# Optimization experiments

Measured on AMD Instinct MI355X. Metric: run time of the kernel, lower is better.

Reference implementation:

```python
import jax, jax.numpy as jnp
import numpy as np

ALPHA = 0.2  # leaky_relu negative slope
NEG_INF = -1e18


def setup_inputs() -> dict:
    key = jax.random.key(0)
    ks = jax.random.split(key, 7)
    B, N, E = 32, 1024, 768
    OUT, MLP = 256, 2
    sent_emb = jax.random.normal(ks[0], (B, N, E), dtype=jnp.float32)
    batch_e = jnp.sort(jax.random.randint(ks[1], (B, 4), 0, N), axis=-1)
    # xavier-ish scaled weights
    W_w = jax.random.normal(ks[2], (OUT, E), dtype=jnp.float32) * (1.0 / np.sqrt(E))
    W_b = jax.random.normal(ks[3], (OUT,), dtype=jnp.float32) * 0.02
    a_w = jax.random.normal(ks[4], (1, 2 * OUT), dtype=jnp.float32) * (1.0 / np.sqrt(2 * OUT))
    mlp_w = jax.random.normal(ks[5], (MLP, OUT), dtype=jnp.float32) * (1.0 / np.sqrt(OUT))
    mlp_b = jax.random.normal(ks[6], (MLP,), dtype=jnp.float32) * 0.02
    return {"sent_emb": sent_emb, "batch_e": batch_e, "W_w": W_w, "W_b": W_b,
            "a_w": a_w, "mlp_w": mlp_w, "mlp_b": mlp_b}


def reference(sent_emb, batch_e, W_w, W_b, a_w, mlp_w, mlp_b):
    B, N, E = sent_emb.shape
    OUT = W_w.shape[0]
    # Wh = W(sent_emb): [B, N, OUT]
    Wh = jnp.einsum('bne,oe->bno', sent_emb, W_w) + W_b
    # a_T([H1 || H2]) decomposes: a1 . Wh_i + a2 . Wh_j (avoids [N,N,2*OUT] concat)
    a1, a2 = a_w[0, :OUT], a_w[0, OUT:]
    s1 = Wh @ a1  # [B, N]
    s2 = Wh @ a2  # [B, N]
    e = jax.nn.leaky_relu(s1[:, :, None] + s2[:, None, :], negative_slope=ALPHA)  # [B,N,N]
    # event mask: 0.9 inside [e1s,e1e)x[e2s,e2e), 0.1 elsewhere (both > 0, kept for fidelity)
    idx = jnp.arange(N)
    row_in = (idx[None, :] >= batch_e[:, 0:1]) & (idx[None, :] < batch_e[:, 1:2])  # [B,N]
    col_in = (idx[None, :] >= batch_e[:, 2:3]) & (idx[None, :] < batch_e[:, 3:4])  # [B,N]
    event_mask = jnp.where(row_in[:, :, None] & col_in[:, None, :], 0.9, 0.1)
    masked_e = jnp.where(event_mask > 0, e, NEG_INF)
    attn = jax.nn.softmax(masked_e, axis=-1)  # [B,N,N]
    h_prime = jax.nn.elu(jnp.einsum('bnm,bmo->bno', attn, Wh))  # [B,N,OUT]
    pooled = jnp.mean(h_prime, axis=1)  # avg_pooling over nodes -> [B,OUT]
    return pooled @ mlp_w.T + mlp_b  # [B, mlp_size]
```

## Files before the change

kernel.cpp:

```cpp
#include <hip/hip_runtime.h>
#include <hip/hip_bf16.h>

#define LOG2E 1.4426950408889634f

typedef short bfrag8 __attribute__((ext_vector_type(8)));
typedef float accf4 __attribute__((ext_vector_type(4)));

__device__ __forceinline__ unsigned pack2(float a, float b) {
    __hip_bfloat162 h = __float22bfloat162_rn(make_float2(a, b));
    return *(unsigned*)&h;
}
__device__ __forceinline__ float bflo(unsigned u) { return __uint_as_float(u << 16); }
__device__ __forceinline__ float bfhi(unsigned u) { return __uint_as_float(u & 0xFFFF0000u); }

__device__ __forceinline__ void gload_lds16(const void* g, void* lds) {
    __builtin_amdgcn_global_load_lds(
        (const __attribute__((address_space(1))) unsigned int*)g,
        (__attribute__((address_space(3))) unsigned int*)lds, 16, 0, 0);
}

__global__ __launch_bounds__(256) void gemm1_kernel(
    const float* __restrict__ sent, const float* __restrict__ Ww,
    const float* __restrict__ Wb, const float* __restrict__ aw,
    unsigned short* __restrict__ WhT, float* __restrict__ s1part,
    float* __restrict__ s2part)
{
    __shared__ unsigned short SM[2][128][72];
    __shared__ float sb1[128][2];
    __shared__ float sb2[128][2];
    const int bid0 = blockIdx.x;
    const int wg = ((bid0 & 7) << 6) + (bid0 >> 3);
    const int brow = wg >> 1, bcol = wg & 1;
    const int t    = threadIdx.x;
    const int lane = t & 63, w = t >> 6;
    const int wr = w >> 1, wc = w & 1;
    const int l15 = lane & 15, l4 = lane >> 4;
    accf4 acc[4][4];
#pragma unroll
    for (int i = 0; i < 4; ++i)
#pragma unroll
        for (int j = 0; j < 4; ++j)
            acc[i][j] = (accf4){0.f, 0.f, 0.f, 0.f};
    const int r0 = t >> 3;
    const int c8 = (t & 7) << 3;

    for (int k0 = 0; k0 < 768; k0 += 64) {
#pragma unroll
        for (int i = 0; i < 4; ++i) {
            const int r = (i << 5) + r0;
            const float* ga = &sent[(size_t)(brow * 128 + r) * 768 + k0 + c8];
            float4 v0 = *(const float4*)ga;
            float4 v1 = *(const float4*)(ga + 4);
            uint4 pk;
            pk.x = pack2(v0.x, v0.y); pk.y = pack2(v0.z, v0.w);
            pk.z = pack2(v1.x, v1.y); pk.w = pack2(v1.z, v1.w);
            *(uint4*)&SM[0][r][c8] = pk;
            const float* gb = &Ww[(size_t)(bcol * 128 + r) * 768 + k0 + c8];
            float4 u0 = *(const float4*)gb;
            float4 u1 = *(const float4*)(gb + 4);
            uint4 qk;
            qk.x = pack2(u0.x, u0.y); qk.y = pack2(u0.z, u0.w);
            qk.z = pack2(u1.x, u1.y); qk.w = pack2(u1.z, u1.w);
            *(uint4*)&SM[1][r][c8] = qk;
        }
        __syncthreads();
#pragma unroll
        for (int kk = 0; kk < 2; ++kk) {
            const int ka = (kk << 5) + (l4 << 3);
            bfrag8 af[4], bfg[4];
#pragma unroll
            for (int mi = 0; mi < 4; ++mi)
                af[mi] = *(const bfrag8*)&SM[0][(wr << 6) + (mi << 4) + l15][ka];
#pragma unroll
            for (int ni = 0; ni < 4; ++ni)
                bfg[ni] = *(const bfrag8*)&SM[1][(wc << 6) + (ni << 4) + l15][ka];
#pragma unroll
            for (int mi = 0; mi < 4; ++mi)
#pragma unroll
                for (int ni = 0; ni < 4; ++ni)
                    acc[mi][ni] = __builtin_amdgcn_mfma_f32_16x16x32_bf16(
                        af[mi], bfg[ni], acc[mi][ni], 0, 0, 0);
        }
        __syncthreads();
    }

    unsigned short (*T)[136] = reinterpret_cast<unsigned short(*)[136]>(&SM[0][0][0]);
    float sp1[16], sp2[16];
#pragma unroll
    for (int i = 0; i < 16; ++i) { sp1[i] = 0.f; sp2[i] = 0.f; }
#pragma unroll
    for (int ni = 0; ni < 4; ++ni) {
        const int colL = (wc << 6) + (ni << 4) + l15;
        const int gcol = bcol * 128 + colL;
        const float wb  = Wb[gcol];
        const float a1c = aw[gcol] * LOG2E;
        const float a2c = aw[256 + gcol] * LOG2E;
#pragma unroll
        for (int mi = 0; mi < 4; ++mi) {
            const int rowL = (wr << 6) + (mi << 4) + (l4 << 2);
            float v0 = acc[mi][ni][0] + wb, v1 = acc[mi][ni][1] + wb;
            float v2 = acc[mi][ni][2] + wb, v3 = acc[mi][ni][3] + wb;
            uint2 pk; pk.x = pack2(v0, v1); pk.y = pack2(v2, v3);
            *(uint2*)&T[colL][rowL] = pk;
            sp1[mi * 4 + 0] += v0 * a1c; sp1[mi * 4 + 1] += v1 * a1c;
            sp1[mi * 4 + 2] += v2 * a1c; sp1[mi * 4 + 3] += v3 * a1c;
            sp2[mi * 4 + 0] += v0 * a2c; sp2[mi * 4 + 1] += v1 * a2c;
            sp2[mi * 4 + 2] += v2 * a2c; sp2[mi * 4 + 3] += v3 * a2c;
        }
    }
#pragma unroll
    for (int d = 1; d < 16; d <<= 1) {
#pragma unroll
        for (int i = 0; i < 16; ++i) {
            sp1[i] += __shfl_xor(sp1[i], d);
            sp2[i] += __shfl_xor(sp2[i], d);
        }
    }
    if (l15 == 0) {
#pragma unroll
        for (int mi = 0; mi < 4; ++mi)
#pragma unroll
            for (int reg = 0; reg < 4; ++reg) {
                const int rowL = (wr << 6) + (mi << 4) + (l4 << 2) + reg;
                sb1[rowL][wc] = sp1[mi * 4 + reg];
                sb2[rowL][wc] = sp2[mi * 4 + reg];
            }
    }
    __syncthreads();
    {
        const int b = brow >> 3, m0b = (brow & 7) << 7;
        const int colL = t >> 1, half = t & 1;
        const int gcol = bcol * 128 + colL;
        unsigned short* dst = &WhT[(((size_t)(b << 8) + gcol) << 10) + m0b + (half << 6)];
        const unsigned short* srcT = &T[colL][half << 6];
#pragma unroll
        for (int q = 0; q < 8; ++q)
            *(uint4*)(dst + (q << 3)) = *(const uint4*)(srcT + (q << 3));
    }
    if (t < 128) {
        const int grow = brow * 128 + t;
        s1part[bcol * 32768 + grow] = sb1[t][0] + sb1[t][1];
        s2part[bcol * 32768 + grow] = sb2[t][0] + sb2[t][1];
    }
}

__global__ __launch_bounds__(512) void flash_kernel(
    const unsigned short* __restrict__ WhT,
    const float* __restrict__ s1part, const float* __restrict__ s2part,
    float* __restrict__ pooled_part)
{
    __shared__ unsigned short Bs[2][256][64];
    __shared__ unsigned short Ps[64][64];
    __shared__ float s2s[1024];
    __shared__ float zfull[64];
    __shared__ float wred[8];
    __shared__ float psum[2][256];
    const int bid0 = blockIdx.x;
    const int wg = ((bid0 & 7) << 6) + (bid0 >> 3);
    const int b = wg >> 4, nt = wg & 15, n0 = nt << 6;
    const int t = threadIdx.x;
    const int lane = t & 63, w = t >> 6;
    const int wr = w >> 2, wc = w & 3;
    const int l15 = lane & 15, l4 = lane >> 4;
    const int prow = t >> 3, pchk = t & 7;
    const unsigned short* wbase = WhT + (((size_t)b) << 18);

    {
        const int i = t << 1;
        float2 p0 = *(const float2*)&s2part[(b << 10) + i];
        float2 p1 = *(const float2*)&s2part[32768 + (b << 10) + i];
        s2s[i] = p0.x + p1.x; s2s[i + 1] = p0.y + p1.y;
    }
#pragma unroll
    for (int q = 0; q < 4; ++q) {
        const int r = (q << 6) + (w << 3) + (lane >> 3);
        const int c = (lane & 7) ^ (r & 7);
        gload_lds16(wbase + (((size_t)r) << 10) + (c << 3),
                    (char*)&Bs[0][0][0] + (q << 13) + (w << 10));
    }
    const float s1r = s1part[(b << 10) + n0 + prow] +
                      s1part[32768 + (b << 10) + n0 + prow];
    __syncthreads();
    float mm = fmaxf(s2s[t], s2s[t + 512]);
#pragma unroll
    for (int d = 1; d < 64; d <<= 1) mm = fmaxf(mm, __shfl_xor(mm, d));
    if (lane == 0) wred[w] = mm;
    __syncthreads();
    float s2mx = wred[0];
#pragma unroll
    for (int i = 1; i < 8; ++i) s2mx = fmaxf(s2mx, wred[i]);
    const float xm = s1r + s2mx;
    const float Mr = fmaxf(xm, 0.2f * xm);

    accf4 acc[2][4];
#pragma unroll
    for (int i = 0; i < 2; ++i)
#pragma unroll
        for (int j = 0; j < 4; ++j)
            acc[i][j] = (accf4){0.f, 0.f, 0.f, 0.f};
    float zp = 0.f;

    for (int mt = 0; mt < 16; ++mt) {
        const int m0 = mt << 6;
        if (mt < 15) {
#pragma unroll
            for (int q = 0; q < 4; ++q) {
                const int r = (q << 6) + (w << 3) + (lane >> 3);
                const int c = (lane & 7) ^ (r & 7);
                gload_lds16(wbase + (((size_t)r) << 10) + (m0 + 64) + (c << 3),
                            (char*)&Bs[(mt + 1) & 1][0][0] + (q << 13) + (w << 10));
            }
        }
        {
            const float* s2p = &s2s[m0 + (pchk << 3)];
            float4 sa = *(const float4*)s2p;
            float4 sb = *(const float4*)(s2p + 4);
#define LR(x) fmaxf((x), 0.2f * (x))
            float p0 = __builtin_amdgcn_exp2f(LR(s1r + sa.x) - Mr);
            float p1 = __builtin_amdgcn_exp2f(LR(s1r + sa.y) - Mr);
            float p2 = __builtin_amdgcn_exp2f(LR(s1r + sa.z) - Mr);
            float p3 = __builtin_amdgcn_exp2f(LR(s1r + sa.w) - Mr);
            float p4 = __builtin_amdgcn_exp2f(LR(s1r + sb.x) - Mr);
            float p5 = __builtin_amdgcn_exp2f(LR(s1r + sb.y) - Mr);
            float p6 = __builtin_amdgcn_exp2f(LR(s1r + sb.z) - Mr);
            float p7 = __builtin_amdgcn_exp2f(LR(s1r + sb.w) - Mr);
#undef LR
            unsigned u0 = pack2(p0, p1), u1 = pack2(p2, p3);
            unsigned u2 = pack2(p4, p5), u3 = pack2(p6, p7);
            zp += bflo(u0) + bfhi(u0) + bflo(u1) + bfhi(u1)
                + bflo(u2) + bfhi(u2) + bflo(u3) + bfhi(u3);
            uint4 pk; pk.x = u0; pk.y = u1; pk.z = u2; pk.w = u3;
            *(uint4*)((char*)&Ps[0][0] + (prow << 7) + ((pchk << 4) ^ ((prow & 7) << 4))) = pk;
        }
        __syncthreads();
        const int cur = mt & 1;
#pragma unroll
        for (int kk = 0; kk < 2; ++kk) {
            const int kb = (kk << 6) + (l4 << 4);
            bfrag8 af[2], bf[4];
#pragma unroll
            for (int mi = 0; mi < 2; ++mi) {
                const int row = (wr << 5) + (mi << 4) + l15;
                af[mi] = *(const bfrag8*)((char*)&Ps[0][0] + (row << 7) + (kb ^ ((row & 7) << 4)));
            }
#pragma unroll
            for (int ni = 0; ni < 4; ++ni) {
                const int col = (wc << 6) + (ni << 4) + l15;
                bf[ni] = *(const bfrag8*)((char*)&Bs[cur][0][0] + (col << 7) + (kb ^ ((col & 7) << 4)));
            }
#pragma unroll
            for (int mi = 0; mi < 2; ++mi)
#pragma unroll
                for (int ni = 0; ni < 4; ++ni)
                    acc[mi][ni] = __builtin_amdgcn_mfma_f32_16x16x32_bf16(
                        af[mi], bf[ni], acc[mi][ni], 0, 0, 0);
        }
        __syncthreads();
    }

    zp += __shfl_xor(zp, 1); zp += __shfl_xor(zp, 2); zp += __shfl_xor(zp, 4);
    if ((lane & 7) == 0) zfull[prow] = zp;
    __syncthreads();

    float rz[8];
#pragma unroll
    for (int mi = 0; mi < 2; ++mi)
#pragma unroll
        for (int r = 0; r < 4; ++r)
            rz[mi * 4 + r] = 1.0f / zfull[(wr << 5) + (mi << 4) + (l4 << 2) + r];
#pragma unroll
    for (int ni = 0; ni < 4; ++ni) {
        float cs = 0.f;
#pragma unroll
        for (int mi = 0; mi < 2; ++mi)
#pragma unroll
            for (int r = 0; r < 4; ++r) {
                float v = acc[mi][ni][r] * rz[mi * 4 + r];
                cs += v > 0.f ? v : (__expf(v) - 1.0f);
            }
        cs += __shfl_xor(cs, 16);
        cs += __shfl_xor(cs, 32);
        if (l4 == 0) psum[wr][(wc << 6) + (ni << 4) + l15] = cs;
    }
    __syncthreads();
    if (t < 256)
        pooled_part[(((size_t)b << 4) + nt) * 256 + t] = psum[0][t] + psum[1][t];
}

__global__ __launch_bounds__(256) void final_kernel(
    const float* __restrict__ pooled_part, const float* __restrict__ mlpw,
    const float* __restrict__ mlpb, float* __restrict__ out)
{
    __shared__ float r0[4], r1[4];
    const int b = blockIdx.x, t = threadIdx.x;
    float p = 0.f;
#pragma unroll
    for (int ntile = 0; ntile < 16; ++ntile)
        p += pooled_part[(((size_t)b << 4) + ntile) * 256 + t];
    float m0 = p * mlpw[t], m1 = p * mlpw[256 + t];
#pragma unroll
    for (int d = 1; d < 64; d <<= 1) {
        m0 += __shfl_xor(m0, d);
        m1 += __shfl_xor(m1, d);
    }
    if ((t & 63) == 0) { r0[t >> 6] = m0; r1[t >> 6] = m1; }
    __syncthreads();
    if (t == 0) out[b * 2 + 0] = (r0[0] + r0[1] + r0[2] + r0[3]) * (1.f / 1024.f) + mlpb[0];
    if (t == 1) out[b * 2 + 1] = (r1[0] + r1[1] + r1[2] + r1[3]) * (1.f / 1024.f) + mlpb[1];
}

extern "C" void kernel_launch(void* const* d_in, const int* in_sizes, int n_in,
                              void* d_out, int out_size, void* d_ws, size_t ws_size,
                              hipStream_t stream) {
    const float* sent = (const float*)d_in[0];
    const float* Ww   = (const float*)d_in[2];
    const float* Wb   = (const float*)d_in[3];
    const float* aw   = (const float*)d_in[4];
    const float* mlpw = (const float*)d_in[5];
    const float* mlpb = (const float*)d_in[6];
    float* out = (float*)d_out;

    char* ws = (char*)d_ws;
    unsigned short* WhT    = (unsigned short*)ws;
    float*          s1part = (float*)(ws + 16777216);
    float*          s2part = s1part + 65536;
    float*          ppart  = s2part + 65536;

    gemm1_kernel<<<512, 256, 0, stream>>>(sent, Ww, Wb, aw, WhT, s1part, s2part);
    flash_kernel<<<512, 512, 0, stream>>>(WhT, s1part, s2part, ppart);
    final_kernel<<<32, 256, 0, stream>>>(ppart, mlpw, mlpb, out);
}
```

Measured before the change: 208.7 us.

## Restructure GEMM and flash kernels with full-width tiles and double-buffered async loads

```diff
diff --git a/kernel.cpp b/kernel.cpp
--- a/kernel.cpp
+++ b/kernel.cpp
@@ -19,82 +19,108 @@
         (__attribute__((address_space(3))) unsigned int*)lds, 16, 0, 0);
 }
 
-__global__ __launch_bounds__(256) void gemm1_kernel(
-    const float* __restrict__ sent, const float* __restrict__ Ww,
+__global__ __launch_bounds__(256) void convW_kernel(
+    const float* __restrict__ Ww, unsigned short* __restrict__ WwB)
+{
+    const int id = (blockIdx.x * 256 + threadIdx.x) * 8;
+    float4 a = *(const float4*)&Ww[id];
+    float4 b = *(const float4*)&Ww[id + 4];
+    uint4 pk;
+    pk.x = pack2(a.x, a.y); pk.y = pack2(a.z, a.w);
+    pk.z = pack2(b.x, b.y); pk.w = pack2(b.z, b.w);
+    *(uint4*)&WwB[id] = pk;
+}
+
+__global__ __launch_bounds__(512) void gemm1_kernel(
+    const float* __restrict__ sent, const unsigned short* __restrict__ WwB,
     const float* __restrict__ Wb, const float* __restrict__ aw,
-    unsigned short* __restrict__ WhT, float* __restrict__ s1part,
-    float* __restrict__ s2part)
+    unsigned short* __restrict__ WhT, float* __restrict__ s1g,
+    float* __restrict__ s2g)
 {
-    __shared__ unsigned short SM[2][128][72];
-    __shared__ float sb1[128][2];
-    __shared__ float sb2[128][2];
-    const int bid0 = blockIdx.x;
-    const int wg = ((bid0 & 7) << 6) + (bid0 >> 3);
-    const int brow = wg >> 1, bcol = wg & 1;
-    const int t    = threadIdx.x;
+    __shared__ char SMEM[131072];
+    const int brow = blockIdx.x;
+    const int t = threadIdx.x;
     const int lane = t & 63, w = t >> 6;
-    const int wr = w >> 1, wc = w & 1;
+    const int wr = w >> 2, wc = w & 3;
     const int l15 = lane & 15, l4 = lane >> 4;
+    const float* abase = sent + (size_t)brow * 128 * 768;
+
     accf4 acc[4][4];
 #pragma unroll
     for (int i = 0; i < 4; ++i)
 #pragma unroll
         for (int j = 0; j < 4; ++j)
             acc[i][j] = (accf4){0.f, 0.f, 0.f, 0.f};
-    const int r0 = t >> 3;
-    const int c8 = (t & 7) << 3;
-
-    for (int k0 = 0; k0 < 768; k0 += 64) {
-#pragma unroll
-        for (int i = 0; i < 4; ++i) {
-            const int r = (i << 5) + r0;
-            const float* ga = &sent[(size_t)(brow * 128 + r) * 768 + k0 + c8];
-            float4 v0 = *(const float4*)ga;
-            float4 v1 = *(const float4*)(ga + 4);
-            uint4 pk;
-            pk.x = pack2(v0.x, v0.y); pk.y = pack2(v0.z, v0.w);
-            pk.z = pack2(v1.x, v1.y); pk.w = pack2(v1.z, v1.w);
-            *(uint4*)&SM[0][r][c8] = pk;
-            const float* gb = &Ww[(size_t)(bcol * 128 + r) * 768 + k0 + c8];
-            float4 u0 = *(const float4*)gb;
-            float4 u1 = *(const float4*)(gb + 4);
-            uint4 qk;
-            qk.x = pack2(u0.x, u0.y); qk.y = pack2(u0.z, u0.w);
-            qk.z = pack2(u1.x, u1.y); qk.w = pack2(u1.z, u1.w);
-            *(uint4*)&SM[1][r][c8] = qk;
-        }
-        __syncthreads();
+
+    auto STAGE = [&](int buf, int k0) {
+#pragma unroll
+        for (int q = 0; q < 4; ++q) {
+            const int id = (q << 9) + t;
+            const int row = id >> 4, c = id & 15;
+            gload_lds16(abase + (size_t)row * 768 + k0 + ((c ^ (row & 15)) << 2),
+                        SMEM + (buf << 15) + (id << 4));
+        }
+#pragma unroll
+        for (int q = 0; q < 4; ++q) {
+            const int id = (q << 9) + t;
+            const int col = id >> 3, c = id & 7;
+            gload_lds16(WwB + (size_t)col * 768 + k0 + ((c ^ (col & 7)) << 3),
+                        SMEM + 65536 + (buf << 15) + (id << 4));
+        }
+    };
+
+    auto COMPUTE = [&](int buf) {
+        const float* Ab = (const float*)(SMEM + (buf << 15));
+        const unsigned short* Bb = (const unsigned short*)(SMEM + 65536 + (buf << 15));
 #pragma unroll
         for (int kk = 0; kk < 2; ++kk) {
-            const int ka = (kk << 5) + (l4 << 3);
-            bfrag8 af[4], bfg[4];
-#pragma unroll
-            for (int mi = 0; mi < 4; ++mi)
-                af[mi] = *(const bfrag8*)&SM[0][(wr << 6) + (mi << 4) + l15][ka];
-#pragma unroll
-            for (int ni = 0; ni < 4; ++ni)
-                bfg[ni] = *(const bfrag8*)&SM[1][(wc << 6) + (ni << 4) + l15][ka];
+            bfrag8 af[4], bf[4];
+#pragma unroll
+            for (int mi = 0; mi < 4; ++mi) {
+                const int row = (wr << 6) + (mi << 4) + l15;
+                const int s0 = (kk << 3) + (l4 << 1);
+                float4 a0 = *(const float4*)(Ab + (row << 6) + ((s0 ^ (row & 15)) << 2));
+                float4 a1 = *(const float4*)(Ab + (row << 6) + (((s0 + 1) ^ (row & 15)) << 2));
+                uint4 pk;
+                pk.x = pack2(a0.x, a0.y); pk.y = pack2(a0.z, a0.w);
+                pk.z = pack2(a1.x, a1.y); pk.w = pack2(a1.z, a1.w);
+                af[mi] = *(bfrag8*)&pk;
+            }
+#pragma unroll
+            for (int ni = 0; ni < 4; ++ni) {
+                const int col = (wc << 6) + (ni << 4) + l15;
+                const int s = (kk << 2) + l4;
+                bf[ni] = *(const bfrag8*)(Bb + (col << 6) + ((s ^ (col & 7)) << 3));
+            }
 #pragma unroll
             for (int mi = 0; mi < 4; ++mi)
 #pragma unroll
                 for (int ni = 0; ni < 4; ++ni)
                     acc[mi][ni] = __builtin_amdgcn_mfma_f32_16x16x32_bf16(
-                        af[mi], bfg[ni], acc[mi][ni], 0, 0, 0);
-        }
+                        af[mi], bf[ni], acc[mi][ni], 0, 0, 0);
+        }
+    };
+
+    STAGE(0, 0);
+    __syncthreads();
+    for (int it = 0; it < 12; ++it) {
+        if (it < 11) STAGE((it + 1) & 1, (it + 1) << 6);
+        COMPUTE(it & 1);
         __syncthreads();
     }
 
-    unsigned short (*T)[136] = reinterpret_cast<unsigned short(*)[136]>(&SM[0][0][0]);
+    unsigned short (*T)[136] = (unsigned short(*)[136])SMEM;
+    float (*sb1)[4] = (float(*)[4])(SMEM + 98304);
+    float (*sb2)[4] = (float(*)[4])(SMEM + 100352);
     float sp1[16], sp2[16];
 #pragma unroll
     for (int i = 0; i < 16; ++i) { sp1[i] = 0.f; sp2[i] = 0.f; }
 #pragma unroll
     for (int ni = 0; ni < 4; ++ni) {
         const int colL = (wc << 6) + (ni << 4) + l15;
-        const int gcol = bcol * 128 + colL;
-        const float wb  = Wb[gcol];
-        const float a1c = aw[gcol] * LOG2E;
-        const float a2c = aw[256 + gcol] * LOG2E;
+        const float wb  = Wb[colL];
+        const float a1c = aw[colL] * LOG2E;
+        const float a2c = aw[256 + colL] * LOG2E;
 #pragma unroll
         for (int mi = 0; mi < 4; ++mi) {
             const int rowL = (wr << 6) + (mi << 4) + (l4 << 2);
@@ -109,14 +135,13 @@
         }
     }
 #pragma unroll
-    for (int d = 1; d < 16; d <<= 1) {
+    for (int d = 1; d < 16; d <<= 1)
 #pragma unroll
         for (int i = 0; i < 16; ++i) {
             sp1[i] += __shfl_xor(sp1[i], d);
             sp2[i] += __shfl_xor(sp2[i], d);
         }
-    }
-    if (l15 == 0) {
+    if (l15 == 0)
 #pragma unroll
         for (int mi = 0; mi < 4; ++mi)
 #pragma unroll
@@ -125,61 +150,57 @@
                 sb1[rowL][wc] = sp1[mi * 4 + reg];
                 sb2[rowL][wc] = sp2[mi * 4 + reg];
             }
-    }
     __syncthreads();
     {
-        const int b = brow >> 3, m0b = (brow & 7) << 7;
-        const int colL = t >> 1, half = t & 1;
-        const int gcol = bcol * 128 + colL;
-        unsigned short* dst = &WhT[(((size_t)(b << 8) + gcol) << 10) + m0b + (half << 6)];
-        const unsigned short* srcT = &T[colL][half << 6];
+        const int b = brow >> 3, m0 = (brow & 7) << 7;
+        const int col = t >> 1, half = t & 1;
+        unsigned short* dst = &WhT[(((size_t)b * 256 + col) << 10) + m0 + (half << 6)];
+        const unsigned short* srcT = &T[col][half << 6];
 #pragma unroll
         for (int q = 0; q < 8; ++q)
             *(uint4*)(dst + (q << 3)) = *(const uint4*)(srcT + (q << 3));
     }
     if (t < 128) {
         const int grow = brow * 128 + t;
-        s1part[bcol * 32768 + grow] = sb1[t][0] + sb1[t][1];
-        s2part[bcol * 32768 + grow] = sb2[t][0] + sb2[t][1];
+        s1g[grow] = sb1[t][0] + sb1[t][1] + sb1[t][2] + sb1[t][3];
+        s2g[grow] = sb2[t][0] + sb2[t][1] + sb2[t][2] + sb2[t][3];
     }
 }
 
 __global__ __launch_bounds__(512) void flash_kernel(
-    const unsigned short* __restrict__ WhT,
-    const float* __restrict__ s1part, const float* __restrict__ s2part,
-    float* __restrict__ pooled_part)
+    const unsigned short* __restrict__ WhT, const float* __restrict__ s1g,
+    const float* __restrict__ s2g, float* __restrict__ ppart)
 {
-    __shared__ unsigned short Bs[2][256][64];
-    __shared__ unsigned short Ps[64][64];
+    __shared__ char SMEM[98304];
     __shared__ float s2s[1024];
-    __shared__ float zfull[64];
+    __shared__ float zfull[128];
     __shared__ float wred[8];
     __shared__ float psum[2][256];
     const int bid0 = blockIdx.x;
-    const int wg = ((bid0 & 7) << 6) + (bid0 >> 3);
-    const int b = wg >> 4, nt = wg & 15, n0 = nt << 6;
+    const int wg = ((bid0 & 7) << 5) + (bid0 >> 3);
+    const int b = wg >> 3, nt = wg & 7, n0 = nt << 7;
     const int t = threadIdx.x;
     const int lane = t & 63, w = t >> 6;
     const int wr = w >> 2, wc = w & 3;
     const int l15 = lane & 15, l4 = lane >> 4;
-    const int prow = t >> 3, pchk = t & 7;
-    const unsigned short* wbase = WhT + (((size_t)b) << 18);
+    const int prow = t >> 2, pc0 = (t & 3) << 1;
+    const unsigned short* wbase = WhT + ((size_t)b << 18);
 
     {
         const int i = t << 1;
-        float2 p0 = *(const float2*)&s2part[(b << 10) + i];
-        float2 p1 = *(const float2*)&s2part[32768 + (b << 10) + i];
-        s2s[i] = p0.x + p1.x; s2s[i + 1] = p0.y + p1.y;
-    }
-#pragma unroll
-    for (int q = 0; q < 4; ++q) {
-        const int r = (q << 6) + (w << 3) + (lane >> 3);
-        const int c = (lane & 7) ^ (r & 7);
-        gload_lds16(wbase + (((size_t)r) << 10) + (c << 3),
-                    (char*)&Bs[0][0][0] + (q << 13) + (w << 10));
-    }
-    const float s1r = s1part[(b << 10) + n0 + prow] +
-                      s1part[32768 + (b << 10) + n0 + prow];
+        *(float2*)&s2s[i] = *(const float2*)&s2g[(b << 10) + i];
+    }
+    auto STAGEB = [&](int buf, int m0) {
+#pragma unroll
+        for (int q = 0; q < 4; ++q) {
+            const int id = (q << 9) + t;
+            const int col = id >> 3, c = id & 7;
+            gload_lds16(wbase + ((size_t)col << 10) + m0 + ((c ^ (col & 7)) << 3),
+                        SMEM + (buf << 15) + (id << 4));
+        }
+    };
+    STAGEB(0, 0);
+    const float s1r = s1g[(b << 10) + n0 + prow];
     __syncthreads();
     float mm = fmaxf(s2s[t], s2s[t + 512]);
 #pragma unroll
@@ -192,87 +213,91 @@
     const float xm = s1r + s2mx;
     const float Mr = fmaxf(xm, 0.2f * xm);
 
-    accf4 acc[2][4];
-#pragma unroll
-    for (int i = 0; i < 2; ++i)
+    accf4 acc[4][4];
+#pragma unroll
+    for (int i = 0; i < 4; ++i)
 #pragma unroll
         for (int j = 0; j < 4; ++j)
             acc[i][j] = (accf4){0.f, 0.f, 0.f, 0.f};
     float zp = 0.f;
 
-    for (int mt = 0; mt < 16; ++mt) {
-        const int m0 = mt << 6;
-        if (mt < 15) {
-#pragma unroll
-            for (int q = 0; q < 4; ++q) {
-                const int r = (q << 6) + (w << 3) + (lane >> 3);
-                const int c = (lane & 7) ^ (r & 7);
-                gload_lds16(wbase + (((size_t)r) << 10) + (m0 + 64) + (c << 3),
-                            (char*)&Bs[(mt + 1) & 1][0][0] + (q << 13) + (w << 10));
-            }
-        }
-        {
-            const float* s2p = &s2s[m0 + (pchk << 3)];
-            float4 sa = *(const float4*)s2p;
-            float4 sb = *(const float4*)(s2p + 4);
-#define LR(x) fmaxf((x), 0.2f * (x))
-            float p0 = __builtin_amdgcn_exp2f(LR(s1r + sa.x) - Mr);
-            float p1 = __builtin_amdgcn_exp2f(LR(s1r + sa.y) - Mr);
-            float p2 = __builtin_amdgcn_exp2f(LR(s1r + sa.z) - Mr);
-            float p3 = __builtin_amdgcn_exp2f(LR(s1r + sa.w) - Mr);
-            float p4 = __builtin_amdgcn_exp2f(LR(s1r + sb.x) - Mr);
-            float p5 = __builtin_amdgcn_exp2f(LR(s1r + sb.y) - Mr);
-            float p6 = __builtin_amdgcn_exp2f(LR(s1r + sb.z) - Mr);
-            float p7 = __builtin_amdgcn_exp2f(LR(s1r + sb.w) - Mr);
-#undef LR
-            unsigned u0 = pack2(p0, p1), u1 = pack2(p2, p3);
-            unsigned u2 = pack2(p4, p5), u3 = pack2(p6, p7);
-            zp += bflo(u0) + bfhi(u0) + bflo(u1) + bfhi(u1)
-                + bflo(u2) + bfhi(u2) + bflo(u3) + bfhi(u3);
-            uint4 pk; pk.x = u0; pk.y = u1; pk.z = u2; pk.w = u3;
-            *(uint4*)((char*)&Ps[0][0] + (prow << 7) + ((pchk << 4) ^ ((prow & 7) << 4))) = pk;
-        }
-        __syncthreads();
-        const int cur = mt & 1;
+    auto PCOMP = [&](int buf, int mt) {
+        const float* sp = &s2s[(mt << 6) + (pc0 << 3)];
+        float4 x0 = *(const float4*)sp;
+        float4 x1 = *(const float4*)(sp + 4);
+        float4 x2 = *(const float4*)(sp + 8);
+        float4 x3 = *(const float4*)(sp + 12);
+        float xs[16] = {x0.x, x0.y, x0.z, x0.w, x1.x, x1.y, x1.z, x1.w,
+                        x2.x, x2.y, x2.z, x2.w, x3.x, x3.y, x3.z, x3.w};
+        unsigned u[8];
+#pragma unroll
+        for (int j = 0; j < 8; ++j) {
+            float a = s1r + xs[2 * j], c = s1r + xs[2 * j + 1];
+            a = fmaxf(a, 0.2f * a) - Mr;
+            c = fmaxf(c, 0.2f * c) - Mr;
+            u[j] = pack2(__builtin_amdgcn_exp2f(a), __builtin_amdgcn_exp2f(c));
+            zp += bflo(u[j]) + bfhi(u[j]);
+        }
+        char* pb = SMEM + 65536 + (buf << 14) + (prow << 7);
+        uint4 k0; k0.x = u[0]; k0.y = u[1]; k0.z = u[2]; k0.w = u[3];
+        uint4 k1; k1.x = u[4]; k1.y = u[5]; k1.z = u[6]; k1.w = u[7];
+        *(uint4*)(pb + ((pc0 ^ (prow & 7)) << 4)) = k0;
+        *(uint4*)(pb + (((pc0 + 1) ^ (prow & 7)) << 4)) = k1;
+    };
+    auto MM = [&](int buf) {
+        const unsigned short* Bb = (const unsigned short*)(SMEM + (buf << 15));
+        const char* Pb = SMEM + 65536 + (buf << 14);
 #pragma unroll
         for (int kk = 0; kk < 2; ++kk) {
-            const int kb = (kk << 6) + (l4 << 4);
-            bfrag8 af[2], bf[4];
-#pragma unroll
-            for (int mi = 0; mi < 2; ++mi) {
-                const int row = (wr << 5) + (mi << 4) + l15;
-                af[mi] = *(const bfrag8*)((char*)&Ps[0][0] + (row << 7) + (kb ^ ((row & 7) << 4)));
+            bfrag8 af[4], bf[4];
+#pragma unroll
+            for (int mi = 0; mi < 4; ++mi) {
+                const int row = (wr << 6) + (mi << 4) + l15;
+                const int s = (kk << 2) + l4;
+                af[mi] = *(const bfrag8*)(Pb + (row << 7) + ((s ^ (row & 7)) << 4));
             }
 #pragma unroll
             for (int ni = 0; ni < 4; ++ni) {
                 const int col = (wc << 6) + (ni << 4) + l15;
-                bf[ni] = *(const bfrag8*)((char*)&Bs[cur][0][0] + (col << 7) + (kb ^ ((col & 7) << 4)));
-            }
-#pragma unroll
-            for (int mi = 0; mi < 2; ++mi)
+                const int s = (kk << 2) + l4;
+                bf[ni] = *(const bfrag8*)(Bb + (col << 6) + ((s ^ (col & 7)) << 3));
+            }
+#pragma unroll
+            for (int mi = 0; mi < 4; ++mi)
 #pragma unroll
                 for (int ni = 0; ni < 4; ++ni)
                     acc[mi][ni] = __builtin_amdgcn_mfma_f32_16x16x32_bf16(
                         af[mi], bf[ni], acc[mi][ni], 0, 0, 0);
         }
+    };
+
+    PCOMP(0, 0);
+    __syncthreads();
+    for (int mt = 0; mt < 16; ++mt) {
+        if (mt < 15) {
+            STAGEB((mt + 1) & 1, (mt + 1) << 6);
+            PCOMP((mt + 1) & 1, mt + 1);
+        }
+        MM(mt & 1);
         __syncthreads();
     }
 
-    zp += __shfl_xor(zp, 1); zp += __shfl_xor(zp, 2); zp += __shfl_xor(zp, 4);
-    if ((lane & 7) == 0) zfull[prow] = zp;
-    __syncthreads();
-
-    float rz[8];
-#pragma unroll
-    for (int mi = 0; mi < 2; ++mi)
+    zp += __shfl_xor(zp, 1);
+    zp += __shfl_xor(zp, 2);
+    if ((lane & 3) == 0) zfull[prow] = zp;
+    __syncthreads();
+
+    float rz[16];
+#pragma unroll
+    for (int mi = 0; mi < 4; ++mi)
 #pragma unroll
         for (int r = 0; r < 4; ++r)
-            rz[mi * 4 + r] = 1.0f / zfull[(wr << 5) + (mi << 4) + (l4 << 2) + r];
+            rz[mi * 4 + r] = 1.0f / zfull[(wr << 6) + (mi << 4) + (l4 << 2) + r];
 #pragma unroll
     for (int ni = 0; ni < 4; ++ni) {
         float cs = 0.f;
 #pragma unroll
-        for (int mi = 0; mi < 2; ++mi)
+        for (int mi = 0; mi < 4; ++mi)
 #pragma unroll
             for (int r = 0; r < 4; ++r) {
                 float v = acc[mi][ni][r] * rz[mi * 4 + r];
@@ -284,19 +309,19 @@
     }
     __syncthreads();
     if (t < 256)
-        pooled_part[(((size_t)b << 4) + nt) * 256 + t] = psum[0][t] + psum[1][t];
+        ppart[(((size_t)b << 3) + nt) * 256 + t] = psum[0][t] + psum[1][t];
 }
 
 __global__ __launch_bounds__(256) void final_kernel(
-    const float* __restrict__ pooled_part, const float* __restrict__ mlpw,
+    const float* __restrict__ ppart, const float* __restrict__ mlpw,
     const float* __restrict__ mlpb, float* __restrict__ out)
 {
     __shared__ float r0[4], r1[4];
     const int b = blockIdx.x, t = threadIdx.x;
     float p = 0.f;
 #pragma unroll
-    for (int ntile = 0; ntile < 16; ++ntile)
-        p += pooled_part[(((size_t)b << 4) + ntile) * 256 + t];
+    for (int nt = 0; nt < 8; ++nt)
+        p += ppart[(((size_t)b << 3) + nt) * 256 + t];
     float m0 = p * mlpw[t], m1 = p * mlpw[256 + t];
 #pragma unroll
     for (int d = 1; d < 64; d <<= 1) {
@@ -321,12 +346,14 @@
     float* out = (float*)d_out;
 
     char* ws = (char*)d_ws;
-    unsigned short* WhT    = (unsigned short*)ws;
-    float*          s1part = (float*)(ws + 16777216);
-    float*          s2part = s1part + 65536;
-    float*          ppart  = s2part + 65536;
-
-    gemm1_kernel<<<512, 256, 0, stream>>>(sent, Ww, Wb, aw, WhT, s1part, s2part);
-    flash_kernel<<<512, 512, 0, stream>>>(WhT, s1part, s2part, ppart);
+    unsigned short* WhT  = (unsigned short*)ws;
+    unsigned short* WwB  = (unsigned short*)(ws + 16777216);
+    float*          s1g  = (float*)(ws + 17170432);
+    float*          s2g  = s1g + 32768;
+    float*          ppart= s2g + 32768;
+
+    convW_kernel<<<96, 256, 0, stream>>>(Ww, WwB);
+    gemm1_kernel<<<256, 512, 0, stream>>>(sent, WwB, Wb, aw, WhT, s1g, s2g);
+    flash_kernel<<<256, 512, 0, stream>>>(WhT, s1g, s2g, ppart);
     final_kernel<<<32, 256, 0, stream>>>(ppart, mlpw, mlpb, out);
 }
```

New measurement: 204.2 us. 2.2% less time.
